# Kernel optimization log

Hardware: AMD Instinct MI355X
Metric: run time of the kernel (lower is better)

## Reference

```python
import jax, jax.numpy as jnp
import numpy as np

FP8_MAX = 448.0  # finfo(float8_e4m3fn).max
G = 128          # quantization block size


def _fp8_roundtrip(x):
    # emulate storage/rounding in float8_e4m3fn
    return x.astype(jnp.float8_e4m3fn).astype(jnp.float32)


def _quant_dequant_act(x, g=G):
    """Dynamic per-token, per-128-column-group fp8 quantization, then dequant.
    Matches fp8_act_quant: scale = amax(group)/FP8_MAX, q = clip(x/scale)."""
    lead, K = x.shape[:-1], x.shape[-1]
    xg = x.reshape(*lead, K // g, g)
    amax = jnp.max(jnp.abs(xg), axis=-1, keepdims=True)
    scale = jnp.maximum(amax, 1e-10) / FP8_MAX
    q = _fp8_roundtrip(jnp.clip(xg / scale, -FP8_MAX, FP8_MAX))
    return (q * scale).reshape(*lead, K)


def _dequant_weight(w, s, g=G):
    """Block-wise dequant: w [E,O,K] fp8 codes (stored as f32), s [E,O/g,K/g] scales."""
    E, O, K = w.shape
    wb = w.reshape(E, O // g, g, K // g, g)
    return (wb * s[:, :, None, :, None]).reshape(E, O, K)


def setup_inputs() -> dict:
    key = jax.random.key(0)
    ks = jax.random.split(key, 7)
    T, H, I, E, TK = 2048, 1024, 512, 16, 4
    hidden_states = jax.random.normal(ks[0], (T, H), dtype=jnp.float32)
    top_k_index = jax.random.randint(ks[1], (T, TK), 0, E)
    top_k_weights = jax.nn.softmax(jax.random.normal(ks[2], (T, TK), dtype=jnp.float32), axis=-1)
    # fp8-representable weight codes + positive block scale grids
    gate_up_proj = _fp8_roundtrip(jax.random.normal(ks[3], (E, 2 * I, H), dtype=jnp.float32) * 8.0)
    gate_up_proj_scale_inv = jax.random.uniform(ks[4], (E, (2 * I) // G, H // G), dtype=jnp.float32,
                                                minval=0.001, maxval=0.005)
    down_proj = _fp8_roundtrip(jax.random.normal(ks[5], (E, H, I), dtype=jnp.float32) * 8.0)
    down_proj_scale_inv = jax.random.uniform(ks[6], (E, H // G, I // G), dtype=jnp.float32,
                                             minval=0.001, maxval=0.005)
    return {
        "hidden_states": hidden_states,
        "top_k_index": top_k_index,
        "top_k_weights": top_k_weights,
        "gate_up_proj": gate_up_proj,
        "gate_up_proj_scale_inv": gate_up_proj_scale_inv,
        "down_proj": down_proj,
        "down_proj_scale_inv": down_proj_scale_inv,
    }


def reference(hidden_states, top_k_index, top_k_weights,
              gate_up_proj, gate_up_proj_scale_inv,
              down_proj, down_proj_scale_inv):
    E = gate_up_proj.shape[0]
    # dynamic activation quant (identical for every expert, since tokens are just gathered rows)
    x_deq = _quant_dequant_act(hidden_states)                       # [T, H]
    w_gu = _dequant_weight(gate_up_proj, gate_up_proj_scale_inv)    # [E, 2I, H]
    w_dn = _dequant_weight(down_proj, down_proj_scale_inv)          # [E, H, I]
    # gate_up GEMM for all experts; tokens not routed to e contribute with weight 0 below
    gate_up = jnp.einsum('th,eoh->teo', x_deq, w_gu)                # [T, E, 2I]
    gate, up = jnp.split(gate_up, 2, axis=-1)
    h = jax.nn.silu(gate) * up                                      # [T, E, I]
    h_deq = _quant_dequant_act(h)                                   # re-quantize intermediate
    expert_out = jnp.einsum('tei,ehi->teh', h_deq, w_dn)            # [T, E, H]
    # routing weight per (token, expert): sum of top_k weights whose index == e
    rw = jnp.einsum('tk,tke->te', top_k_weights,
                    jax.nn.one_hot(top_k_index, E, dtype=hidden_states.dtype))
    return jnp.einsum('teh,te->th', expert_out, rw)                 # [T, H] float32 accumulation
```

## Files before the change

kernel.cpp:

```cpp
#include <hip/hip_runtime.h>
#include <math.h>

#define T_TOK 2048
#define H_DIM 1024
#define I_DIM 512
#define N_EXP 16
#define TOPK  4
#define NPAIR (T_TOK*TOPK)

typedef unsigned short u16;
typedef __attribute__((ext_vector_type(8))) short s8v;
typedef __attribute__((ext_vector_type(4))) float f4v;

#define GLDS(g, l) __builtin_amdgcn_global_load_lds( \
    (const __attribute__((address_space(1))) void*)(g), \
    (__attribute__((address_space(3))) void*)(l), 16, 0, 0)

__device__ __forceinline__ float fp8_rt(float v) {
    float av = fabsf(v);
    if (av < 0.015625f) {
        return rintf(v * 512.0f) * 0.001953125f;
    }
    unsigned u = __float_as_uint(v);
    unsigned lsb = (u >> 20) & 1u;
    u = (u + 0x7FFFFu + lsb) & 0xFFF00000u;
    return __uint_as_float(u);
}

__device__ __forceinline__ u16 f2bf(float v) {
    return (u16)(__float_as_uint(v) >> 16);
}

__global__ void k_cvt(const float* __restrict__ in, u16* __restrict__ out, int n8) {
    int i = blockIdx.x * 256 + threadIdx.x;
    if (i >= n8) return;
    const float4* p = (const float4*)in + (size_t)i * 2;
    float4 a = p[0], b = p[1];
    int4 st;
    st.x = (int)((unsigned)f2bf(a.x) | ((unsigned)f2bf(a.y) << 16));
    st.y = (int)((unsigned)f2bf(a.z) | ((unsigned)f2bf(a.w) << 16));
    st.z = (int)((unsigned)f2bf(b.x) | ((unsigned)f2bf(b.y) << 16));
    st.w = (int)((unsigned)f2bf(b.z) | ((unsigned)f2bf(b.w) << 16));
    ((int4*)out)[i] = st;
}

__global__ void k_quant_x(const float* __restrict__ x, u16* __restrict__ xq,
                          float* __restrict__ xs) {
    int t = blockIdx.x, tid = threadIdx.x;
    float4 v = ((const float4*)(x + (size_t)t * H_DIM))[tid];
    float a = fmaxf(fmaxf(fabsf(v.x), fabsf(v.y)), fmaxf(fabsf(v.z), fabsf(v.w)));
    #pragma unroll
    for (int m = 16; m >= 1; m >>= 1) a = fmaxf(a, __shfl_xor(a, m));
    float s = fmaxf(a, 1e-10f) / 448.0f;
    ushort4 r;
    r.x = f2bf(fp8_rt(fminf(fmaxf(v.x / s, -448.f), 448.f)));
    r.y = f2bf(fp8_rt(fminf(fmaxf(v.y / s, -448.f), 448.f)));
    r.z = f2bf(fp8_rt(fminf(fmaxf(v.z / s, -448.f), 448.f)));
    r.w = f2bf(fp8_rt(fminf(fmaxf(v.w / s, -448.f), 448.f)));
    ((ushort4*)(xq + (size_t)t * H_DIM))[tid] = r;
    if ((tid & 31) == 0) xs[t * 8 + (tid >> 5)] = s;
}

__global__ void k_route(const int* __restrict__ idx, int* __restrict__ counts,
                        int* __restrict__ lists) {
    int p = blockIdx.x * 256 + threadIdx.x;
    if (p < NPAIR) {
        int e = idx[p];
        int pos = atomicAdd(&counts[e], 1);
        lists[e * NPAIR + pos] = p;
    }
}

__global__ __launch_bounds__(256, 3)
void k_gateup(const u16* __restrict__ xq, const float* __restrict__ xs,
              const int* __restrict__ counts, const int* __restrict__ lists,
              const u16* __restrict__ wgu, const float* __restrict__ sgu,
              const u16* __restrict__ zbuf, float* __restrict__ hbuf) {
    int bid = blockIdx.x;
    int e = bid & 15, tile = bid >> 4;
    int tt = tile >> 3, it = tile & 7;
    int n = counts[e];
    if (tt * 64 >= n) return;

    __shared__ __align__(16) u16 sm[2][12288];
    __shared__ float xs_l[64][8];
    __shared__ int ptok[64];

    int tid = threadIdx.x;
    int w = tid >> 6, lane = tid & 63;
    int m = w & 1, q = w >> 1;
    int l15 = lane & 15, l4 = lane >> 4;

    if (tid < 64) {
        int slot = tt * 64 + tid;
        ptok[tid] = (slot < n) ? lists[e * NPAIR + slot] : -1;
    }
    __syncthreads();
    {
        int r = tid >> 2, kb4 = (tid & 3) * 2;
        int p = ptok[r];
        xs_l[r][kb4]     = (p >= 0) ? xs[(p >> 2) * 8 + kb4]     : 0.f;
        xs_l[r][kb4 + 1] = (p >= 0) ? xs[(p >> 2) * 8 + kb4 + 1] : 0.f;
    }

    const u16* wbase = wgu + (size_t)e * 1024 * 1024;
    const u16* srcB[4];
    #pragma unroll
    for (int j = 0; j < 4; ++j) {
        int s = j * 256 + tid;
        int row = s >> 3, c = s & 7, cg = c ^ (row & 7);
        int nrow = (row < 64) ? it * 64 + row : 448 + it * 64 + row;
        srcB[j] = wbase + (size_t)nrow * H_DIM + cg * 8;
    }
    const u16* srcA[2];
    #pragma unroll
    for (int j = 0; j < 2; ++j) {
        int s = j * 256 + tid;
        int row = s >> 3, c = s & 7, cg = c ^ (row & 7);
        int p = ptok[row];
        srcA[j] = (p >= 0) ? xq + (size_t)(p >> 2) * H_DIM + cg * 8 : zbuf;
    }

    int idxA[2][2], idxB[4][2];
    #pragma unroll
    for (int fm = 0; fm < 2; ++fm) {
        int ar = m * 32 + fm * 16 + l15;
        #pragma unroll
        for (int kg = 0; kg < 2; ++kg)
            idxA[fm][kg] = 8192 + ar * 64 + (((kg * 4 + l4) ^ (ar & 7)) * 8);
    }
    #pragma unroll
    for (int nf = 0; nf < 4; ++nf) {
        int br = q * 64 + nf * 16 + l15;
        #pragma unroll
        for (int kg = 0; kg < 2; ++kg)
            idxB[nf][kg] = br * 64 + (((kg * 4 + l4) ^ (br & 7)) * 8);
    }

    auto stage = [&](int buf) {
        #pragma unroll
        for (int j = 0; j < 4; ++j) { GLDS(srcB[j], &sm[buf][j * 2048 + tid * 8]); srcB[j] += 64; }
        #pragma unroll
        for (int j = 0; j < 2; ++j) { GLDS(srcA[j], &sm[buf][8192 + j * 2048 + tid * 8]); srcA[j] += 64; }
    };

    f4v master[2][4], part[2][4];
    #pragma unroll
    for (int a = 0; a < 2; ++a)
        #pragma unroll
        for (int b = 0; b < 4; ++b) { master[a][b] = (f4v){0,0,0,0}; part[a][b] = (f4v){0,0,0,0}; }

    const float* swp = sgu + e * 64 + (q ? 4 + (it >> 1) : (it >> 1)) * 8;

    stage(0);
    __syncthreads();

    for (int t = 0; t < 16; ++t) {
        if (t < 15) stage((t + 1) & 1);
        const u16* buf = &sm[t & 1][0];
        #pragma unroll
        for (int kg = 0; kg < 2; ++kg) {
            s8v a0 = *(const s8v*)&buf[idxA[0][kg]];
            s8v a1 = *(const s8v*)&buf[idxA[1][kg]];
            #pragma unroll
            for (int nf = 0; nf < 4; ++nf) {
                s8v b = *(const s8v*)&buf[idxB[nf][kg]];
                part[0][nf] = __builtin_amdgcn_mfma_f32_16x16x32_bf16(a0, b, part[0][nf], 0, 0, 0);
                part[1][nf] = __builtin_amdgcn_mfma_f32_16x16x32_bf16(a1, b, part[1][nf], 0, 0, 0);
            }
        }
        if (t & 1) {
            int kb = t >> 1;
            float sw = swp[kb];
            #pragma unroll
            for (int fm = 0; fm < 2; ++fm) {
                float c0 = xs_l[m * 32 + fm * 16 + l4 * 4 + 0][kb] * sw;
                float c1 = xs_l[m * 32 + fm * 16 + l4 * 4 + 1][kb] * sw;
                float c2 = xs_l[m * 32 + fm * 16 + l4 * 4 + 2][kb] * sw;
                float c3 = xs_l[m * 32 + fm * 16 + l4 * 4 + 3][kb] * sw;
                #pragma unroll
                for (int nf = 0; nf < 4; ++nf) {
                    master[fm][nf][0] += c0 * part[fm][nf][0];
                    master[fm][nf][1] += c1 * part[fm][nf][1];
                    master[fm][nf][2] += c2 * part[fm][nf][2];
                    master[fm][nf][3] += c3 * part[fm][nf][3];
                    part[fm][nf] = (f4v){0,0,0,0};
                }
            }
        }
        __syncthreads();
    }

    float* Ul = (float*)sm;
    if (q == 1) {
        #pragma unroll
        for (int fm = 0; fm < 2; ++fm)
            #pragma unroll
            for (int nf = 0; nf < 4; ++nf)
                #pragma unroll
                for (int r = 0; r < 4; ++r)
                    Ul[(m * 32 + fm * 16 + l4 * 4 + r) * 65 + nf * 16 + l15] = master[fm][nf][r];
    }
    __syncthreads();
    if (q == 0) {
        #pragma unroll
        for (int fm = 0; fm < 2; ++fm)
            #pragma unroll
            for (int r = 0; r < 4; ++r) {
                int row = m * 32 + fm * 16 + l4 * 4 + r;
                int p = ptok[row];
                if (p < 0) continue;
                float* drow = hbuf + (size_t)p * I_DIM + it * 64;
                #pragma unroll
                for (int nf = 0; nf < 4; ++nf) {
                    float g = master[fm][nf][r];
                    float u = Ul[row * 65 + nf * 16 + l15];
                    drow[nf * 16 + l15] = (g / (1.0f + expf(-g))) * u;
                }
            }
    }
}

__global__ void k_quant_h(const float* __restrict__ h, u16* __restrict__ hq,
                          float* __restrict__ hs) {
    int p = blockIdx.x, tid = threadIdx.x;
    float4 v = ((const float4*)(h + (size_t)p * I_DIM))[tid];
    float a = fmaxf(fmaxf(fabsf(v.x), fabsf(v.y)), fmaxf(fabsf(v.z), fabsf(v.w)));
    #pragma unroll
    for (int m = 16; m >= 1; m >>= 1) a = fmaxf(a, __shfl_xor(a, m));
    float s = fmaxf(a, 1e-10f) / 448.0f;
    ushort4 r;
    r.x = f2bf(fp8_rt(fminf(fmaxf(v.x / s, -448.f), 448.f)));
    r.y = f2bf(fp8_rt(fminf(fmaxf(v.y / s, -448.f), 448.f)));
    r.z = f2bf(fp8_rt(fminf(fmaxf(v.z / s, -448.f), 448.f)));
    r.w = f2bf(fp8_rt(fminf(fmaxf(v.w / s, -448.f), 448.f)));
    ((ushort4*)(hq + (size_t)p * I_DIM))[tid] = r;
    if ((tid & 31) == 0) hs[p * 4 + (tid >> 5)] = s;
}

__global__ __launch_bounds__(256, 3)
void k_down(const u16* __restrict__ hq, const float* __restrict__ hs,
            const int* __restrict__ counts, const int* __restrict__ lists,
            const u16* __restrict__ wdn, const float* __restrict__ sdn,
            const float* __restrict__ tkw, const u16* __restrict__ zbuf,
            float* __restrict__ dout) {
    int bid = blockIdx.x;
    int e = bid & 15, tile = bid >> 4;
    int tt = tile >> 3, nt = tile & 7;
    int n = counts[e];
    if (tt * 64 >= n) return;

    __shared__ __align__(16) u16 sm[2][12288];
    __shared__ float hs_l[64][4];
    __shared__ float rw_l[64];
    __shared__ int ptok[64];

    int tid = threadIdx.x;
    int w = tid >> 6, lane = tid & 63;
    int m = w & 1, q = w >> 1;
    int l15 = lane & 15, l4 = lane >> 4;

    if (tid < 64) {
        int slot = tt * 64 + tid;
        ptok[tid] = (slot < n) ? lists[e * NPAIR + slot] : -1;
    }
    __syncthreads();
    {
        int r = tid >> 2, kb = tid & 3;
        int p = ptok[r];
        hs_l[r][kb] = (p >= 0) ? hs[p * 4 + kb] : 0.f;
        if (tid < 64) rw_l[tid] = (ptok[tid] >= 0) ? tkw[ptok[tid]] : 0.f;
    }

    const u16* wbase = wdn + (size_t)e * H_DIM * I_DIM;
    const u16* srcB[4];
    #pragma unroll
    for (int j = 0; j < 4; ++j) {
        int s = j * 256 + tid;
        int row = s >> 3, c = s & 7, cg = c ^ (row & 7);
        srcB[j] = wbase + (size_t)(nt * 128 + row) * I_DIM + cg * 8;
    }
    const u16* srcA[2];
    #pragma unroll
    for (int j = 0; j < 2; ++j) {
        int s = j * 256 + tid;
        int row = s >> 3, c = s & 7, cg = c ^ (row & 7);
        int p = ptok[row];
        srcA[j] = (p >= 0) ? hq + (size_t)p * I_DIM + cg * 8 : zbuf;
    }

    int idxA[2][2], idxB[4][2];
    #pragma unroll
    for (int fm = 0; fm < 2; ++fm) {
        int ar = m * 32 + fm * 16 + l15;
        #pragma unroll
        for (int kg = 0; kg < 2; ++kg)
            idxA[fm][kg] = 8192 + ar * 64 + (((kg * 4 + l4) ^ (ar & 7)) * 8);
    }
    #pragma unroll
    for (int nf = 0; nf < 4; ++nf) {
        int br = q * 64 + nf * 16 + l15;
        #pragma unroll
        for (int kg = 0; kg < 2; ++kg)
            idxB[nf][kg] = br * 64 + (((kg * 4 + l4) ^ (br & 7)) * 8);
    }

    auto stage = [&](int buf) {
        #pragma unroll
        for (int j = 0; j < 4; ++j) { GLDS(srcB[j], &sm[buf][j * 2048 + tid * 8]); srcB[j] += 64; }
        #pragma unroll
        for (int j = 0; j < 2; ++j) { GLDS(srcA[j], &sm[buf][8192 + j * 2048 + tid * 8]); srcA[j] += 64; }
    };

    f4v master[2][4], part[2][4];
    #pragma unroll
    for (int a = 0; a < 2; ++a)
        #pragma unroll
        for (int b = 0; b < 4; ++b) { master[a][b] = (f4v){0,0,0,0}; part[a][b] = (f4v){0,0,0,0}; }

    const float* swp = sdn + (e * 8 + nt) * 4;

    stage(0);
    __syncthreads();

    for (int t = 0; t < 8; ++t) {
        if (t < 7) stage((t + 1) & 1);
        const u16* buf = &sm[t & 1][0];
        #pragma unroll
        for (int kg = 0; kg < 2; ++kg) {
            s8v a0 = *(const s8v*)&buf[idxA[0][kg]];
            s8v a1 = *(const s8v*)&buf[idxA[1][kg]];
            #pragma unroll
            for (int nf = 0; nf < 4; ++nf) {
                s8v b = *(const s8v*)&buf[idxB[nf][kg]];
                part[0][nf] = __builtin_amdgcn_mfma_f32_16x16x32_bf16(a0, b, part[0][nf], 0, 0, 0);
                part[1][nf] = __builtin_amdgcn_mfma_f32_16x16x32_bf16(a1, b, part[1][nf], 0, 0, 0);
            }
        }
        if (t & 1) {
            int kb = t >> 1;
            float sw = swp[kb];
            #pragma unroll
            for (int fm = 0; fm < 2; ++fm) {
                float c0 = hs_l[m * 32 + fm * 16 + l4 * 4 + 0][kb] * sw;
                float c1 = hs_l[m * 32 + fm * 16 + l4 * 4 + 1][kb] * sw;
                float c2 = hs_l[m * 32 + fm * 16 + l4 * 4 + 2][kb] * sw;
                float c3 = hs_l[m * 32 + fm * 16 + l4 * 4 + 3][kb] * sw;
                #pragma unroll
                for (int nf = 0; nf < 4; ++nf) {
                    master[fm][nf][0] += c0 * part[fm][nf][0];
                    master[fm][nf][1] += c1 * part[fm][nf][1];
                    master[fm][nf][2] += c2 * part[fm][nf][2];
                    master[fm][nf][3] += c3 * part[fm][nf][3];
                    part[fm][nf] = (f4v){0,0,0,0};
                }
            }
        }
        __syncthreads();
    }

    #pragma unroll
    for (int fm = 0; fm < 2; ++fm)
        #pragma unroll
        for (int r = 0; r < 4; ++r) {
            int row = m * 32 + fm * 16 + l4 * 4 + r;
            int p = ptok[row];
            if (p < 0) continue;
            float rw = rw_l[row];
            float* drow = dout + (size_t)p * H_DIM + nt * 128 + q * 64;
            #pragma unroll
            for (int nf = 0; nf < 4; ++nf)
                drow[nf * 16 + l15] = rw * master[fm][nf][r];
        }
}

__global__ void k_reduce(const float* __restrict__ dout, float* __restrict__ out) {
    int i = blockIdx.x * 256 + threadIdx.x;
    int t = i >> 8, h4 = i & 255;
    const float4* d = (const float4*)dout;
    float4 a = d[(size_t)(t * 4 + 0) * 256 + h4];
    float4 b = d[(size_t)(t * 4 + 1) * 256 + h4];
    float4 c = d[(size_t)(t * 4 + 2) * 256 + h4];
    float4 e = d[(size_t)(t * 4 + 3) * 256 + h4];
    float4 r;
    r.x = a.x + b.x + c.x + e.x;
    r.y = a.y + b.y + c.y + e.y;
    r.z = a.z + b.z + c.z + e.z;
    r.w = a.w + b.w + c.w + e.w;
    ((float4*)out)[i] = r;
}

extern "C" void kernel_launch(void* const* d_in, const int* in_sizes, int n_in,
                              void* d_out, int out_size, void* d_ws, size_t ws_size,
                              hipStream_t stream) {
    const float* hs_in = (const float*)d_in[0];
    const int*   tki = (const int*)d_in[1];
    const float* tkw = (const float*)d_in[2];
    const float* wgu = (const float*)d_in[3];
    const float* sgu = (const float*)d_in[4];
    const float* wdn = (const float*)d_in[5];
    const float* sdn = (const float*)d_in[6];
    float* out = (float*)d_out;

    char* ws = (char*)d_ws;
    const size_t MB = 1024 * 1024;
    u16*   wgu_bf = (u16*)(ws);
    float* dout   = (float*)(ws);
    u16*   wdn_bf = (u16*)(ws + 32 * MB);
    u16*   xq     = (u16*)(ws + 48 * MB);
    float* xs     = (float*)(ws + 52 * MB);
    float* hbuf   = (float*)(ws + 53 * MB);
    u16*   hq     = (u16*)(ws + 69 * MB);
    float* hs     = (float*)(ws + 77 * MB);
    int*   counts = (int*)(ws + 78 * MB);
    u16*   zbuf   = (u16*)(ws + 78 * MB + 4096);
    int*   lists  = (int*)(ws + 78 * MB + 65536);

    hipMemsetAsync(counts, 0, 256, stream);
    hipMemsetAsync(zbuf, 0, 4096, stream);

    k_cvt<<<8192, 256, 0, stream>>>(wgu, wgu_bf, N_EXP * 2 * I_DIM * H_DIM / 8);
    k_cvt<<<4096, 256, 0, stream>>>(wdn, wdn_bf, N_EXP * H_DIM * I_DIM / 8);
    k_quant_x<<<T_TOK, 256, 0, stream>>>(hs_in, xq, xs);
    k_route<<<NPAIR / 256, 256, 0, stream>>>(tki, counts, lists);
    k_gateup<<<2048, 256, 0, stream>>>(xq, xs, counts, lists, wgu_bf, sgu, zbuf, hbuf);
    k_quant_h<<<NPAIR, 128, 0, stream>>>(hbuf, hq, hs);
    k_down<<<2048, 256, 0, stream>>>(hq, hs, counts, lists, wdn_bf, sdn, tkw, zbuf, dout);
    k_reduce<<<T_TOK * H_DIM / 1024, 256, 0, stream>>>(dout, out);
}
```

Baseline: 255.4 us.

## Fuse fp32-to-bf16 weight conversion into GEMM staging, drop convert kernels

Removes the standalone weight conversion kernels and instead loads fp32 weights into registers in the gate-up and down GEMMs, converting to bf16 and writing swizzled into LDS after the compute of each step. Activation tiles still use direct global-to-LDS loads. MFMA sections get raised wave priority. This avoids a full extra pass writing and re-reading converted weights, at the cost of doubling weight bytes per tile load and more registers, and redundant conversion across token tiles.

```diff
diff --git a/kernel.cpp b/kernel.cpp
--- a/kernel.cpp
+++ b/kernel.cpp
@@ -27,21 +27,8 @@
     return __uint_as_float(u);
 }
 
-__device__ __forceinline__ u16 f2bf(float v) {
-    return (u16)(__float_as_uint(v) >> 16);
-}
-
-__global__ void k_cvt(const float* __restrict__ in, u16* __restrict__ out, int n8) {
-    int i = blockIdx.x * 256 + threadIdx.x;
-    if (i >= n8) return;
-    const float4* p = (const float4*)in + (size_t)i * 2;
-    float4 a = p[0], b = p[1];
-    int4 st;
-    st.x = (int)((unsigned)f2bf(a.x) | ((unsigned)f2bf(a.y) << 16));
-    st.y = (int)((unsigned)f2bf(a.z) | ((unsigned)f2bf(a.w) << 16));
-    st.z = (int)((unsigned)f2bf(b.x) | ((unsigned)f2bf(b.y) << 16));
-    st.w = (int)((unsigned)f2bf(b.z) | ((unsigned)f2bf(b.w) << 16));
-    ((int4*)out)[i] = st;
+__device__ __forceinline__ unsigned f2bf(float v) {
+    return __float_as_uint(v) >> 16;
 }
 
 __global__ void k_quant_x(const float* __restrict__ x, u16* __restrict__ xq,
@@ -53,10 +40,10 @@
     for (int m = 16; m >= 1; m >>= 1) a = fmaxf(a, __shfl_xor(a, m));
     float s = fmaxf(a, 1e-10f) / 448.0f;
     ushort4 r;
-    r.x = f2bf(fp8_rt(fminf(fmaxf(v.x / s, -448.f), 448.f)));
-    r.y = f2bf(fp8_rt(fminf(fmaxf(v.y / s, -448.f), 448.f)));
-    r.z = f2bf(fp8_rt(fminf(fmaxf(v.z / s, -448.f), 448.f)));
-    r.w = f2bf(fp8_rt(fminf(fmaxf(v.w / s, -448.f), 448.f)));
+    r.x = (u16)f2bf(fp8_rt(fminf(fmaxf(v.x / s, -448.f), 448.f)));
+    r.y = (u16)f2bf(fp8_rt(fminf(fmaxf(v.y / s, -448.f), 448.f)));
+    r.z = (u16)f2bf(fp8_rt(fminf(fmaxf(v.z / s, -448.f), 448.f)));
+    r.w = (u16)f2bf(fp8_rt(fminf(fmaxf(v.w / s, -448.f), 448.f)));
     ((ushort4*)(xq + (size_t)t * H_DIM))[tid] = r;
     if ((tid & 31) == 0) xs[t * 8 + (tid >> 5)] = s;
 }
@@ -74,7 +61,7 @@
 __global__ __launch_bounds__(256, 3)
 void k_gateup(const u16* __restrict__ xq, const float* __restrict__ xs,
               const int* __restrict__ counts, const int* __restrict__ lists,
-              const u16* __restrict__ wgu, const float* __restrict__ sgu,
+              const float* __restrict__ wgu, const float* __restrict__ sgu,
               const u16* __restrict__ zbuf, float* __restrict__ hbuf) {
     int bid = blockIdx.x;
     int e = bid & 15, tile = bid >> 4;
@@ -103,14 +90,14 @@
         xs_l[r][kb4 + 1] = (p >= 0) ? xs[(p >> 2) * 8 + kb4 + 1] : 0.f;
     }
 
-    const u16* wbase = wgu + (size_t)e * 1024 * 1024;
-    const u16* srcB[4];
+    const float* wf = wgu + (size_t)e * (2 * I_DIM) * H_DIM;
+    int srow = tid >> 3, sc = tid & 7;
+    int nrowj[4]; int dstB[4];
     #pragma unroll
     for (int j = 0; j < 4; ++j) {
-        int s = j * 256 + tid;
-        int row = s >> 3, c = s & 7, cg = c ^ (row & 7);
-        int nrow = (row < 64) ? it * 64 + row : 448 + it * 64 + row;
-        srcB[j] = wbase + (size_t)nrow * H_DIM + cg * 8;
+        int row = j * 32 + srow;
+        nrowj[j] = (row < 64) ? it * 64 + row : 448 + it * 64 + row;
+        dstB[j] = row * 64 + (sc ^ (srow & 7)) * 8;
     }
     const u16* srcA[2];
     #pragma unroll
@@ -137,11 +124,28 @@
             idxB[nf][kg] = br * 64 + (((kg * 4 + l4) ^ (br & 7)) * 8);
     }
 
-    auto stage = [&](int buf) {
-        #pragma unroll
-        for (int j = 0; j < 4; ++j) { GLDS(srcB[j], &sm[buf][j * 2048 + tid * 8]); srcB[j] += 64; }
-        #pragma unroll
-        for (int j = 0; j < 2; ++j) { GLDS(srcA[j], &sm[buf][8192 + j * 2048 + tid * 8]); srcA[j] += 64; }
+    float4 brg[8];
+    auto loadB = [&](int ck) {
+        #pragma unroll
+        for (int j = 0; j < 4; ++j) {
+            const float4* p = (const float4*)(wf + (size_t)nrowj[j] * H_DIM + ck * 64 + sc * 8);
+            brg[2 * j] = p[0]; brg[2 * j + 1] = p[1];
+        }
+    };
+    auto writeB = [&](int buf) {
+        #pragma unroll
+        for (int j = 0; j < 4; ++j) {
+            int4 st;
+            st.x = (int)(f2bf(brg[2*j].x)   | (f2bf(brg[2*j].y)   << 16));
+            st.y = (int)(f2bf(brg[2*j].z)   | (f2bf(brg[2*j].w)   << 16));
+            st.z = (int)(f2bf(brg[2*j+1].x) | (f2bf(brg[2*j+1].y) << 16));
+            st.w = (int)(f2bf(brg[2*j+1].z) | (f2bf(brg[2*j+1].w) << 16));
+            *(int4*)&sm[buf][dstB[j]] = st;
+        }
+    };
+    auto stageA = [&](int buf, int ck) {
+        #pragma unroll
+        for (int j = 0; j < 2; ++j) GLDS(srcA[j] + ck * 64, &sm[buf][8192 + j * 2048 + tid * 8]);
     };
 
     f4v master[2][4], part[2][4];
@@ -152,12 +156,13 @@
 
     const float* swp = sgu + e * 64 + (q ? 4 + (it >> 1) : (it >> 1)) * 8;
 
-    stage(0);
+    loadB(0); stageA(0, 0); writeB(0);
     __syncthreads();
 
     for (int t = 0; t < 16; ++t) {
-        if (t < 15) stage((t + 1) & 1);
+        if (t < 15) { loadB(t + 1); stageA((t + 1) & 1, t + 1); }
         const u16* buf = &sm[t & 1][0];
+        __builtin_amdgcn_s_setprio(1);
         #pragma unroll
         for (int kg = 0; kg < 2; ++kg) {
             s8v a0 = *(const s8v*)&buf[idxA[0][kg]];
@@ -169,6 +174,7 @@
                 part[1][nf] = __builtin_amdgcn_mfma_f32_16x16x32_bf16(a1, b, part[1][nf], 0, 0, 0);
             }
         }
+        __builtin_amdgcn_s_setprio(0);
         if (t & 1) {
             int kb = t >> 1;
             float sw = swp[kb];
@@ -188,6 +194,7 @@
                 }
             }
         }
+        if (t < 15) writeB((t + 1) & 1);
         __syncthreads();
     }
 
@@ -230,10 +237,10 @@
     for (int m = 16; m >= 1; m >>= 1) a = fmaxf(a, __shfl_xor(a, m));
     float s = fmaxf(a, 1e-10f) / 448.0f;
     ushort4 r;
-    r.x = f2bf(fp8_rt(fminf(fmaxf(v.x / s, -448.f), 448.f)));
-    r.y = f2bf(fp8_rt(fminf(fmaxf(v.y / s, -448.f), 448.f)));
-    r.z = f2bf(fp8_rt(fminf(fmaxf(v.z / s, -448.f), 448.f)));
-    r.w = f2bf(fp8_rt(fminf(fmaxf(v.w / s, -448.f), 448.f)));
+    r.x = (u16)f2bf(fp8_rt(fminf(fmaxf(v.x / s, -448.f), 448.f)));
+    r.y = (u16)f2bf(fp8_rt(fminf(fmaxf(v.y / s, -448.f), 448.f)));
+    r.z = (u16)f2bf(fp8_rt(fminf(fmaxf(v.z / s, -448.f), 448.f)));
+    r.w = (u16)f2bf(fp8_rt(fminf(fmaxf(v.w / s, -448.f), 448.f)));
     ((ushort4*)(hq + (size_t)p * I_DIM))[tid] = r;
     if ((tid & 31) == 0) hs[p * 4 + (tid >> 5)] = s;
 }
@@ -241,7 +248,7 @@
 __global__ __launch_bounds__(256, 3)
 void k_down(const u16* __restrict__ hq, const float* __restrict__ hs,
             const int* __restrict__ counts, const int* __restrict__ lists,
-            const u16* __restrict__ wdn, const float* __restrict__ sdn,
+            const float* __restrict__ wdn, const float* __restrict__ sdn,
             const float* __restrict__ tkw, const u16* __restrict__ zbuf,
             float* __restrict__ dout) {
     int bid = blockIdx.x;
@@ -272,13 +279,14 @@
         if (tid < 64) rw_l[tid] = (ptok[tid] >= 0) ? tkw[ptok[tid]] : 0.f;
     }
 
-    const u16* wbase = wdn + (size_t)e * H_DIM * I_DIM;
-    const u16* srcB[4];
+    const float* wf = wdn + (size_t)e * H_DIM * I_DIM;
+    int srow = tid >> 3, sc = tid & 7;
+    int nrowj[4]; int dstB[4];
     #pragma unroll
     for (int j = 0; j < 4; ++j) {
-        int s = j * 256 + tid;
-        int row = s >> 3, c = s & 7, cg = c ^ (row & 7);
-        srcB[j] = wbase + (size_t)(nt * 128 + row) * I_DIM + cg * 8;
+        int row = j * 32 + srow;
+        nrowj[j] = nt * 128 + row;
+        dstB[j] = row * 64 + (sc ^ (srow & 7)) * 8;
     }
     const u16* srcA[2];
     #pragma unroll
@@ -305,11 +313,28 @@
             idxB[nf][kg] = br * 64 + (((kg * 4 + l4) ^ (br & 7)) * 8);
     }
 
-    auto stage = [&](int buf) {
-        #pragma unroll
-        for (int j = 0; j < 4; ++j) { GLDS(srcB[j], &sm[buf][j * 2048 + tid * 8]); srcB[j] += 64; }
-        #pragma unroll
-        for (int j = 0; j < 2; ++j) { GLDS(srcA[j], &sm[buf][8192 + j * 2048 + tid * 8]); srcA[j] += 64; }
+    float4 brg[8];
+    auto loadB = [&](int ck) {
+        #pragma unroll
+        for (int j = 0; j < 4; ++j) {
+            const float4* p = (const float4*)(wf + (size_t)nrowj[j] * I_DIM + ck * 64 + sc * 8);
+            brg[2 * j] = p[0]; brg[2 * j + 1] = p[1];
+        }
+    };
+    auto writeB = [&](int buf) {
+        #pragma unroll
+        for (int j = 0; j < 4; ++j) {
+            int4 st;
+            st.x = (int)(f2bf(brg[2*j].x)   | (f2bf(brg[2*j].y)   << 16));
+            st.y = (int)(f2bf(brg[2*j].z)   | (f2bf(brg[2*j].w)   << 16));
+            st.z = (int)(f2bf(brg[2*j+1].x) | (f2bf(brg[2*j+1].y) << 16));
+            st.w = (int)(f2bf(brg[2*j+1].z) | (f2bf(brg[2*j+1].w) << 16));
+            *(int4*)&sm[buf][dstB[j]] = st;
+        }
+    };
+    auto stageA = [&](int buf, int ck) {
+        #pragma unroll
+        for (int j = 0; j < 2; ++j) GLDS(srcA[j] + ck * 64, &sm[buf][8192 + j * 2048 + tid * 8]);
     };
 
     f4v master[2][4], part[2][4];
@@ -320,12 +345,13 @@
 
     const float* swp = sdn + (e * 8 + nt) * 4;
 
-    stage(0);
+    loadB(0); stageA(0, 0); writeB(0);
     __syncthreads();
 
     for (int t = 0; t < 8; ++t) {
-        if (t < 7) stage((t + 1) & 1);
+        if (t < 7) { loadB(t + 1); stageA((t + 1) & 1, t + 1); }
         const u16* buf = &sm[t & 1][0];
+        __builtin_amdgcn_s_setprio(1);
         #pragma unroll
         for (int kg = 0; kg < 2; ++kg) {
             s8v a0 = *(const s8v*)&buf[idxA[0][kg]];
@@ -337,6 +363,7 @@
                 part[1][nf] = __builtin_amdgcn_mfma_f32_16x16x32_bf16(a1, b, part[1][nf], 0, 0, 0);
             }
         }
+        __builtin_amdgcn_s_setprio(0);
         if (t & 1) {
             int kb = t >> 1;
             float sw = swp[kb];
@@ -356,6 +383,7 @@
                 }
             }
         }
+        if (t < 7) writeB((t + 1) & 1);
         __syncthreads();
     }
 
@@ -404,9 +432,7 @@
 
     char* ws = (char*)d_ws;
     const size_t MB = 1024 * 1024;
-    u16*   wgu_bf = (u16*)(ws);
     float* dout   = (float*)(ws);
-    u16*   wdn_bf = (u16*)(ws + 32 * MB);
     u16*   xq     = (u16*)(ws + 48 * MB);
     float* xs     = (float*)(ws + 52 * MB);
     float* hbuf   = (float*)(ws + 53 * MB);
@@ -419,12 +445,10 @@
     hipMemsetAsync(counts, 0, 256, stream);
     hipMemsetAsync(zbuf, 0, 4096, stream);
 
-    k_cvt<<<8192, 256, 0, stream>>>(wgu, wgu_bf, N_EXP * 2 * I_DIM * H_DIM / 8);
-    k_cvt<<<4096, 256, 0, stream>>>(wdn, wdn_bf, N_EXP * H_DIM * I_DIM / 8);
     k_quant_x<<<T_TOK, 256, 0, stream>>>(hs_in, xq, xs);
     k_route<<<NPAIR / 256, 256, 0, stream>>>(tki, counts, lists);
-    k_gateup<<<2048, 256, 0, stream>>>(xq, xs, counts, lists, wgu_bf, sgu, zbuf, hbuf);
+    k_gateup<<<2048, 256, 0, stream>>>(xq, xs, counts, lists, wgu, sgu, zbuf, hbuf);
     k_quant_h<<<NPAIR, 128, 0, stream>>>(hbuf, hq, hs);
-    k_down<<<2048, 256, 0, stream>>>(hq, hs, counts, lists, wdn_bf, sdn, tkw, zbuf, dout);
+    k_down<<<2048, 256, 0, stream>>>(hq, hs, counts, lists, wdn, sdn, tkw, zbuf, dout);
     k_reduce<<<T_TOK * H_DIM / 1024, 256, 0, stream>>>(dout, out);
 }
```

After: 279.0 us. 9.2% more time.

## Enlarge MoE GEMM token tile to 128 rows and merge weight conversion kernels

Applied to the files above, without the earlier changes.

The gate-up and down expert GEMM kernels now process 128 routed tokens per block instead of 64. Each wave computes a 64x64 output tile with 4x4 MFMA fragments, so weight tiles staged in LDS are reused across twice as many tokens. This halves the grid and lowers occupancy bounds to 2 blocks per CU because of higher register and LDS use. Separately, the two fp32-to-bf16 weight conversion launches are merged into one kernel that picks its source by index, saving a launch.

```diff
diff --git a/kernel.cpp b/kernel.cpp
--- a/kernel.cpp
+++ b/kernel.cpp
@@ -27,20 +27,23 @@
     return __uint_as_float(u);
 }
 
-__device__ __forceinline__ u16 f2bf(float v) {
-    return (u16)(__float_as_uint(v) >> 16);
-}
-
-__global__ void k_cvt(const float* __restrict__ in, u16* __restrict__ out, int n8) {
+__device__ __forceinline__ unsigned f2bf(float v) {
+    return __float_as_uint(v) >> 16;
+}
+
+#define N8_GU (N_EXP * 2 * I_DIM * H_DIM / 8)
+__global__ void k_cvt(const float* __restrict__ a, u16* __restrict__ oa,
+                      const float* __restrict__ b, u16* __restrict__ ob) {
     int i = blockIdx.x * 256 + threadIdx.x;
-    if (i >= n8) return;
+    const float* in = a; u16* out = oa;
+    if (i >= N8_GU) { in = b; out = ob; i -= N8_GU; }
     const float4* p = (const float4*)in + (size_t)i * 2;
-    float4 a = p[0], b = p[1];
+    float4 x = p[0], y = p[1];
     int4 st;
-    st.x = (int)((unsigned)f2bf(a.x) | ((unsigned)f2bf(a.y) << 16));
-    st.y = (int)((unsigned)f2bf(a.z) | ((unsigned)f2bf(a.w) << 16));
-    st.z = (int)((unsigned)f2bf(b.x) | ((unsigned)f2bf(b.y) << 16));
-    st.w = (int)((unsigned)f2bf(b.z) | ((unsigned)f2bf(b.w) << 16));
+    st.x = (int)(f2bf(x.x) | (f2bf(x.y) << 16));
+    st.y = (int)(f2bf(x.z) | (f2bf(x.w) << 16));
+    st.z = (int)(f2bf(y.x) | (f2bf(y.y) << 16));
+    st.w = (int)(f2bf(y.z) | (f2bf(y.w) << 16));
     ((int4*)out)[i] = st;
 }
 
@@ -53,10 +56,10 @@
     for (int m = 16; m >= 1; m >>= 1) a = fmaxf(a, __shfl_xor(a, m));
     float s = fmaxf(a, 1e-10f) / 448.0f;
     ushort4 r;
-    r.x = f2bf(fp8_rt(fminf(fmaxf(v.x / s, -448.f), 448.f)));
-    r.y = f2bf(fp8_rt(fminf(fmaxf(v.y / s, -448.f), 448.f)));
-    r.z = f2bf(fp8_rt(fminf(fmaxf(v.z / s, -448.f), 448.f)));
-    r.w = f2bf(fp8_rt(fminf(fmaxf(v.w / s, -448.f), 448.f)));
+    r.x = (u16)f2bf(fp8_rt(fminf(fmaxf(v.x / s, -448.f), 448.f)));
+    r.y = (u16)f2bf(fp8_rt(fminf(fmaxf(v.y / s, -448.f), 448.f)));
+    r.z = (u16)f2bf(fp8_rt(fminf(fmaxf(v.z / s, -448.f), 448.f)));
+    r.w = (u16)f2bf(fp8_rt(fminf(fmaxf(v.w / s, -448.f), 448.f)));
     ((ushort4*)(xq + (size_t)t * H_DIM))[tid] = r;
     if ((tid & 31) == 0) xs[t * 8 + (tid >> 5)] = s;
 }
@@ -71,7 +74,7 @@
     }
 }
 
-__global__ __launch_bounds__(256, 3)
+__global__ __launch_bounds__(256, 2)
 void k_gateup(const u16* __restrict__ xq, const float* __restrict__ xs,
               const int* __restrict__ counts, const int* __restrict__ lists,
               const u16* __restrict__ wgu, const float* __restrict__ sgu,
@@ -80,27 +83,28 @@
     int e = bid & 15, tile = bid >> 4;
     int tt = tile >> 3, it = tile & 7;
     int n = counts[e];
-    if (tt * 64 >= n) return;
-
-    __shared__ __align__(16) u16 sm[2][12288];
-    __shared__ float xs_l[64][8];
-    __shared__ int ptok[64];
+    if (tt * 128 >= n) return;
+
+    __shared__ __align__(16) u16 sm[2][16384];
+    __shared__ float xs_l[128][8];
+    __shared__ int ptok[128];
 
     int tid = threadIdx.x;
     int w = tid >> 6, lane = tid & 63;
-    int m = w & 1, q = w >> 1;
+    int wr = w & 1, wc = w >> 1;
     int l15 = lane & 15, l4 = lane >> 4;
 
-    if (tid < 64) {
-        int slot = tt * 64 + tid;
+    if (tid < 128) {
+        int slot = tt * 128 + tid;
         ptok[tid] = (slot < n) ? lists[e * NPAIR + slot] : -1;
     }
     __syncthreads();
     {
-        int r = tid >> 2, kb4 = (tid & 3) * 2;
+        int base = tid * 4, r = base >> 3, kb = base & 7;
         int p = ptok[r];
-        xs_l[r][kb4]     = (p >= 0) ? xs[(p >> 2) * 8 + kb4]     : 0.f;
-        xs_l[r][kb4 + 1] = (p >= 0) ? xs[(p >> 2) * 8 + kb4 + 1] : 0.f;
+        #pragma unroll
+        for (int i = 0; i < 4; ++i)
+            xs_l[r][kb + i] = (p >= 0) ? xs[(p >> 2) * 8 + kb + i] : 0.f;
     }
 
     const u16* wbase = wgu + (size_t)e * 1024 * 1024;
@@ -112,79 +116,78 @@
         int nrow = (row < 64) ? it * 64 + row : 448 + it * 64 + row;
         srcB[j] = wbase + (size_t)nrow * H_DIM + cg * 8;
     }
-    const u16* srcA[2];
-    #pragma unroll
-    for (int j = 0; j < 2; ++j) {
+    const u16* srcA[4];
+    #pragma unroll
+    for (int j = 0; j < 4; ++j) {
         int s = j * 256 + tid;
         int row = s >> 3, c = s & 7, cg = c ^ (row & 7);
         int p = ptok[row];
         srcA[j] = (p >= 0) ? xq + (size_t)(p >> 2) * H_DIM + cg * 8 : zbuf;
     }
 
-    int idxA[2][2], idxB[4][2];
-    #pragma unroll
-    for (int fm = 0; fm < 2; ++fm) {
-        int ar = m * 32 + fm * 16 + l15;
+    int idxA[4][2], idxB[4][2];
+    #pragma unroll
+    for (int fr = 0; fr < 4; ++fr) {
+        int ar = wr * 64 + fr * 16 + l15;
         #pragma unroll
         for (int kg = 0; kg < 2; ++kg)
-            idxA[fm][kg] = 8192 + ar * 64 + (((kg * 4 + l4) ^ (ar & 7)) * 8);
-    }
-    #pragma unroll
-    for (int nf = 0; nf < 4; ++nf) {
-        int br = q * 64 + nf * 16 + l15;
+            idxA[fr][kg] = 8192 + ar * 64 + (((kg * 4 + l4) ^ (ar & 7)) * 8);
+    }
+    #pragma unroll
+    for (int nc = 0; nc < 4; ++nc) {
+        int br = wc * 64 + nc * 16 + l15;
         #pragma unroll
         for (int kg = 0; kg < 2; ++kg)
-            idxB[nf][kg] = br * 64 + (((kg * 4 + l4) ^ (br & 7)) * 8);
-    }
-
-    auto stage = [&](int buf) {
-        #pragma unroll
-        for (int j = 0; j < 4; ++j) { GLDS(srcB[j], &sm[buf][j * 2048 + tid * 8]); srcB[j] += 64; }
-        #pragma unroll
-        for (int j = 0; j < 2; ++j) { GLDS(srcA[j], &sm[buf][8192 + j * 2048 + tid * 8]); srcA[j] += 64; }
+            idxB[nc][kg] = br * 64 + (((kg * 4 + l4) ^ (br & 7)) * 8);
+    }
+
+    auto stage = [&](int buf, int ck) {
+        #pragma unroll
+        for (int j = 0; j < 4; ++j) GLDS(srcB[j] + ck * 64, &sm[buf][(j * 256 + tid) * 8]);
+        #pragma unroll
+        for (int j = 0; j < 4; ++j) GLDS(srcA[j] + ck * 64, &sm[buf][8192 + (j * 256 + tid) * 8]);
     };
 
-    f4v master[2][4], part[2][4];
-    #pragma unroll
-    for (int a = 0; a < 2; ++a)
+    f4v master[4][4], part[4][4];
+    #pragma unroll
+    for (int a = 0; a < 4; ++a)
         #pragma unroll
         for (int b = 0; b < 4; ++b) { master[a][b] = (f4v){0,0,0,0}; part[a][b] = (f4v){0,0,0,0}; }
 
-    const float* swp = sgu + e * 64 + (q ? 4 + (it >> 1) : (it >> 1)) * 8;
-
-    stage(0);
+    const float* swp = sgu + e * 64 + (wc ? 4 + (it >> 1) : (it >> 1)) * 8;
+
+    stage(0, 0);
     __syncthreads();
 
     for (int t = 0; t < 16; ++t) {
-        if (t < 15) stage((t + 1) & 1);
+        if (t < 15) stage((t + 1) & 1, t + 1);
         const u16* buf = &sm[t & 1][0];
         #pragma unroll
         for (int kg = 0; kg < 2; ++kg) {
-            s8v a0 = *(const s8v*)&buf[idxA[0][kg]];
-            s8v a1 = *(const s8v*)&buf[idxA[1][kg]];
-            #pragma unroll
-            for (int nf = 0; nf < 4; ++nf) {
-                s8v b = *(const s8v*)&buf[idxB[nf][kg]];
-                part[0][nf] = __builtin_amdgcn_mfma_f32_16x16x32_bf16(a0, b, part[0][nf], 0, 0, 0);
-                part[1][nf] = __builtin_amdgcn_mfma_f32_16x16x32_bf16(a1, b, part[1][nf], 0, 0, 0);
+            s8v a[4];
+            #pragma unroll
+            for (int fr = 0; fr < 4; ++fr) a[fr] = *(const s8v*)&buf[idxA[fr][kg]];
+            #pragma unroll
+            for (int nc = 0; nc < 4; ++nc) {
+                s8v b = *(const s8v*)&buf[idxB[nc][kg]];
+                #pragma unroll
+                for (int fr = 0; fr < 4; ++fr)
+                    part[fr][nc] = __builtin_amdgcn_mfma_f32_16x16x32_bf16(a[fr], b, part[fr][nc], 0, 0, 0);
             }
         }
         if (t & 1) {
             int kb = t >> 1;
             float sw = swp[kb];
             #pragma unroll
-            for (int fm = 0; fm < 2; ++fm) {
-                float c0 = xs_l[m * 32 + fm * 16 + l4 * 4 + 0][kb] * sw;
-                float c1 = xs_l[m * 32 + fm * 16 + l4 * 4 + 1][kb] * sw;
-                float c2 = xs_l[m * 32 + fm * 16 + l4 * 4 + 2][kb] * sw;
-                float c3 = xs_l[m * 32 + fm * 16 + l4 * 4 + 3][kb] * sw;
-                #pragma unroll
-                for (int nf = 0; nf < 4; ++nf) {
-                    master[fm][nf][0] += c0 * part[fm][nf][0];
-                    master[fm][nf][1] += c1 * part[fm][nf][1];
-                    master[fm][nf][2] += c2 * part[fm][nf][2];
-                    master[fm][nf][3] += c3 * part[fm][nf][3];
-                    part[fm][nf] = (f4v){0,0,0,0};
+            for (int fr = 0; fr < 4; ++fr) {
+                #pragma unroll
+                for (int r = 0; r < 4; ++r) {
+                    float c = xs_l[wr * 64 + fr * 16 + l4 * 4 + r][kb] * sw;
+                    #pragma unroll
+                    for (int nc = 0; nc < 4; ++nc) {
+                        master[fr][nc][r] += c * part[fr][nc][r];
+                        part[fr][nc][r] = 0.f;
+                    }
                 }
             }
         }
@@ -192,30 +195,30 @@
     }
 
     float* Ul = (float*)sm;
-    if (q == 1) {
-        #pragma unroll
-        for (int fm = 0; fm < 2; ++fm)
-            #pragma unroll
-            for (int nf = 0; nf < 4; ++nf)
+    if (wc == 1) {
+        #pragma unroll
+        for (int fr = 0; fr < 4; ++fr)
+            #pragma unroll
+            for (int nc = 0; nc < 4; ++nc)
                 #pragma unroll
                 for (int r = 0; r < 4; ++r)
-                    Ul[(m * 32 + fm * 16 + l4 * 4 + r) * 65 + nf * 16 + l15] = master[fm][nf][r];
+                    Ul[(wr * 64 + fr * 16 + l4 * 4 + r) * 66 + nc * 16 + l15] = master[fr][nc][r];
     }
     __syncthreads();
-    if (q == 0) {
-        #pragma unroll
-        for (int fm = 0; fm < 2; ++fm)
+    if (wc == 0) {
+        #pragma unroll
+        for (int fr = 0; fr < 4; ++fr)
             #pragma unroll
             for (int r = 0; r < 4; ++r) {
-                int row = m * 32 + fm * 16 + l4 * 4 + r;
+                int row = wr * 64 + fr * 16 + l4 * 4 + r;
                 int p = ptok[row];
                 if (p < 0) continue;
                 float* drow = hbuf + (size_t)p * I_DIM + it * 64;
                 #pragma unroll
-                for (int nf = 0; nf < 4; ++nf) {
-                    float g = master[fm][nf][r];
-                    float u = Ul[row * 65 + nf * 16 + l15];
-                    drow[nf * 16 + l15] = (g / (1.0f + expf(-g))) * u;
+                for (int nc = 0; nc < 4; ++nc) {
+                    float g = master[fr][nc][r];
+                    float u = Ul[row * 66 + nc * 16 + l15];
+                    drow[nc * 16 + l15] = (g / (1.0f + expf(-g))) * u;
                 }
             }
     }
@@ -230,15 +233,15 @@
     for (int m = 16; m >= 1; m >>= 1) a = fmaxf(a, __shfl_xor(a, m));
     float s = fmaxf(a, 1e-10f) / 448.0f;
     ushort4 r;
-    r.x = f2bf(fp8_rt(fminf(fmaxf(v.x / s, -448.f), 448.f)));
-    r.y = f2bf(fp8_rt(fminf(fmaxf(v.y / s, -448.f), 448.f)));
-    r.z = f2bf(fp8_rt(fminf(fmaxf(v.z / s, -448.f), 448.f)));
-    r.w = f2bf(fp8_rt(fminf(fmaxf(v.w / s, -448.f), 448.f)));
+    r.x = (u16)f2bf(fp8_rt(fminf(fmaxf(v.x / s, -448.f), 448.f)));
+    r.y = (u16)f2bf(fp8_rt(fminf(fmaxf(v.y / s, -448.f), 448.f)));
+    r.z = (u16)f2bf(fp8_rt(fminf(fmaxf(v.z / s, -448.f), 448.f)));
+    r.w = (u16)f2bf(fp8_rt(fminf(fmaxf(v.w / s, -448.f), 448.f)));
     ((ushort4*)(hq + (size_t)p * I_DIM))[tid] = r;
     if ((tid & 31) == 0) hs[p * 4 + (tid >> 5)] = s;
 }
 
-__global__ __launch_bounds__(256, 3)
+__global__ __launch_bounds__(256, 2)
 void k_down(const u16* __restrict__ hq, const float* __restrict__ hs,
             const int* __restrict__ counts, const int* __restrict__ lists,
             const u16* __restrict__ wdn, const float* __restrict__ sdn,
@@ -248,28 +251,29 @@
     int e = bid & 15, tile = bid >> 4;
     int tt = tile >> 3, nt = tile & 7;
     int n = counts[e];
-    if (tt * 64 >= n) return;
-
-    __shared__ __align__(16) u16 sm[2][12288];
-    __shared__ float hs_l[64][4];
-    __shared__ float rw_l[64];
-    __shared__ int ptok[64];
+    if (tt * 128 >= n) return;
+
+    __shared__ __align__(16) u16 sm[2][16384];
+    __shared__ float hs_l[128][4];
+    __shared__ float rw_l[128];
+    __shared__ int ptok[128];
 
     int tid = threadIdx.x;
     int w = tid >> 6, lane = tid & 63;
-    int m = w & 1, q = w >> 1;
+    int wr = w & 1, wc = w >> 1;
     int l15 = lane & 15, l4 = lane >> 4;
 
-    if (tid < 64) {
-        int slot = tt * 64 + tid;
+    if (tid < 128) {
+        int slot = tt * 128 + tid;
         ptok[tid] = (slot < n) ? lists[e * NPAIR + slot] : -1;
     }
     __syncthreads();
     {
-        int r = tid >> 2, kb = tid & 3;
+        int base = tid * 2, r = base >> 2, kb = base & 3;
         int p = ptok[r];
-        hs_l[r][kb] = (p >= 0) ? hs[p * 4 + kb] : 0.f;
-        if (tid < 64) rw_l[tid] = (ptok[tid] >= 0) ? tkw[ptok[tid]] : 0.f;
+        hs_l[r][kb]     = (p >= 0) ? hs[p * 4 + kb]     : 0.f;
+        hs_l[r][kb + 1] = (p >= 0) ? hs[p * 4 + kb + 1] : 0.f;
+        if (tid < 128) rw_l[tid] = (ptok[tid] >= 0) ? tkw[ptok[tid]] : 0.f;
     }
 
     const u16* wbase = wdn + (size_t)e * H_DIM * I_DIM;
@@ -280,79 +284,78 @@
         int row = s >> 3, c = s & 7, cg = c ^ (row & 7);
         srcB[j] = wbase + (size_t)(nt * 128 + row) * I_DIM + cg * 8;
     }
-    const u16* srcA[2];
-    #pragma unroll
-    for (int j = 0; j < 2; ++j) {
+    const u16* srcA[4];
+    #pragma unroll
+    for (int j = 0; j < 4; ++j) {
         int s = j * 256 + tid;
         int row = s >> 3, c = s & 7, cg = c ^ (row & 7);
         int p = ptok[row];
         srcA[j] = (p >= 0) ? hq + (size_t)p * I_DIM + cg * 8 : zbuf;
     }
 
-    int idxA[2][2], idxB[4][2];
-    #pragma unroll
-    for (int fm = 0; fm < 2; ++fm) {
-        int ar = m * 32 + fm * 16 + l15;
+    int idxA[4][2], idxB[4][2];
+    #pragma unroll
+    for (int fr = 0; fr < 4; ++fr) {
+        int ar = wr * 64 + fr * 16 + l15;
         #pragma unroll
         for (int kg = 0; kg < 2; ++kg)
-            idxA[fm][kg] = 8192 + ar * 64 + (((kg * 4 + l4) ^ (ar & 7)) * 8);
-    }
-    #pragma unroll
-    for (int nf = 0; nf < 4; ++nf) {
-        int br = q * 64 + nf * 16 + l15;
+            idxA[fr][kg] = 8192 + ar * 64 + (((kg * 4 + l4) ^ (ar & 7)) * 8);
+    }
+    #pragma unroll
+    for (int nc = 0; nc < 4; ++nc) {
+        int br = wc * 64 + nc * 16 + l15;
         #pragma unroll
         for (int kg = 0; kg < 2; ++kg)
-            idxB[nf][kg] = br * 64 + (((kg * 4 + l4) ^ (br & 7)) * 8);
-    }
-
-    auto stage = [&](int buf) {
-        #pragma unroll
-        for (int j = 0; j < 4; ++j) { GLDS(srcB[j], &sm[buf][j * 2048 + tid * 8]); srcB[j] += 64; }
-        #pragma unroll
-        for (int j = 0; j < 2; ++j) { GLDS(srcA[j], &sm[buf][8192 + j * 2048 + tid * 8]); srcA[j] += 64; }
+            idxB[nc][kg] = br * 64 + (((kg * 4 + l4) ^ (br & 7)) * 8);
+    }
+
+    auto stage = [&](int buf, int ck) {
+        #pragma unroll
+        for (int j = 0; j < 4; ++j) GLDS(srcB[j] + ck * 64, &sm[buf][(j * 256 + tid) * 8]);
+        #pragma unroll
+        for (int j = 0; j < 4; ++j) GLDS(srcA[j] + ck * 64, &sm[buf][8192 + (j * 256 + tid) * 8]);
     };
 
-    f4v master[2][4], part[2][4];
-    #pragma unroll
-    for (int a = 0; a < 2; ++a)
+    f4v master[4][4], part[4][4];
+    #pragma unroll
+    for (int a = 0; a < 4; ++a)
         #pragma unroll
         for (int b = 0; b < 4; ++b) { master[a][b] = (f4v){0,0,0,0}; part[a][b] = (f4v){0,0,0,0}; }
 
     const float* swp = sdn + (e * 8 + nt) * 4;
 
-    stage(0);
+    stage(0, 0);
     __syncthreads();
 
     for (int t = 0; t < 8; ++t) {
-        if (t < 7) stage((t + 1) & 1);
+        if (t < 7) stage((t + 1) & 1, t + 1);
         const u16* buf = &sm[t & 1][0];
         #pragma unroll
         for (int kg = 0; kg < 2; ++kg) {
-            s8v a0 = *(const s8v*)&buf[idxA[0][kg]];
-            s8v a1 = *(const s8v*)&buf[idxA[1][kg]];
-            #pragma unroll
-            for (int nf = 0; nf < 4; ++nf) {
-                s8v b = *(const s8v*)&buf[idxB[nf][kg]];
-                part[0][nf] = __builtin_amdgcn_mfma_f32_16x16x32_bf16(a0, b, part[0][nf], 0, 0, 0);
-                part[1][nf] = __builtin_amdgcn_mfma_f32_16x16x32_bf16(a1, b, part[1][nf], 0, 0, 0);
+            s8v a[4];
+            #pragma unroll
+            for (int fr = 0; fr < 4; ++fr) a[fr] = *(const s8v*)&buf[idxA[fr][kg]];
+            #pragma unroll
+            for (int nc = 0; nc < 4; ++nc) {
+                s8v b = *(const s8v*)&buf[idxB[nc][kg]];
+                #pragma unroll
+                for (int fr = 0; fr < 4; ++fr)
+                    part[fr][nc] = __builtin_amdgcn_mfma_f32_16x16x32_bf16(a[fr], b, part[fr][nc], 0, 0, 0);
             }
         }
         if (t & 1) {
             int kb = t >> 1;
             float sw = swp[kb];
             #pragma unroll
-            for (int fm = 0; fm < 2; ++fm) {
-                float c0 = hs_l[m * 32 + fm * 16 + l4 * 4 + 0][kb] * sw;
-                float c1 = hs_l[m * 32 + fm * 16 + l4 * 4 + 1][kb] * sw;
-                float c2 = hs_l[m * 32 + fm * 16 + l4 * 4 + 2][kb] * sw;
-                float c3 = hs_l[m * 32 + fm * 16 + l4 * 4 + 3][kb] * sw;
-                #pragma unroll
-                for (int nf = 0; nf < 4; ++nf) {
-                    master[fm][nf][0] += c0 * part[fm][nf][0];
-                    master[fm][nf][1] += c1 * part[fm][nf][1];
-                    master[fm][nf][2] += c2 * part[fm][nf][2];
-                    master[fm][nf][3] += c3 * part[fm][nf][3];
-                    part[fm][nf] = (f4v){0,0,0,0};
+            for (int fr = 0; fr < 4; ++fr) {
+                #pragma unroll
+                for (int r = 0; r < 4; ++r) {
+                    float c = hs_l[wr * 64 + fr * 16 + l4 * 4 + r][kb] * sw;
+                    #pragma unroll
+                    for (int nc = 0; nc < 4; ++nc) {
+                        master[fr][nc][r] += c * part[fr][nc][r];
+                        part[fr][nc][r] = 0.f;
+                    }
                 }
             }
         }
@@ -360,17 +363,17 @@
     }
 
     #pragma unroll
-    for (int fm = 0; fm < 2; ++fm)
+    for (int fr = 0; fr < 4; ++fr)
         #pragma unroll
         for (int r = 0; r < 4; ++r) {
-            int row = m * 32 + fm * 16 + l4 * 4 + r;
+            int row = wr * 64 + fr * 16 + l4 * 4 + r;
             int p = ptok[row];
             if (p < 0) continue;
             float rw = rw_l[row];
-            float* drow = dout + (size_t)p * H_DIM + nt * 128 + q * 64;
-            #pragma unroll
-            for (int nf = 0; nf < 4; ++nf)
-                drow[nf * 16 + l15] = rw * master[fm][nf][r];
+            float* drow = dout + (size_t)p * H_DIM + nt * 128 + wc * 64;
+            #pragma unroll
+            for (int nc = 0; nc < 4; ++nc)
+                drow[nc * 16 + l15] = rw * master[fr][nc][r];
         }
 }
 
@@ -419,12 +422,11 @@
     hipMemsetAsync(counts, 0, 256, stream);
     hipMemsetAsync(zbuf, 0, 4096, stream);
 
-    k_cvt<<<8192, 256, 0, stream>>>(wgu, wgu_bf, N_EXP * 2 * I_DIM * H_DIM / 8);
-    k_cvt<<<4096, 256, 0, stream>>>(wdn, wdn_bf, N_EXP * H_DIM * I_DIM / 8);
+    k_cvt<<<12288, 256, 0, stream>>>(wgu, wgu_bf, wdn, wdn_bf);
     k_quant_x<<<T_TOK, 256, 0, stream>>>(hs_in, xq, xs);
     k_route<<<NPAIR / 256, 256, 0, stream>>>(tki, counts, lists);
-    k_gateup<<<2048, 256, 0, stream>>>(xq, xs, counts, lists, wgu_bf, sgu, zbuf, hbuf);
+    k_gateup<<<1024, 256, 0, stream>>>(xq, xs, counts, lists, wgu_bf, sgu, zbuf, hbuf);
     k_quant_h<<<NPAIR, 128, 0, stream>>>(hbuf, hq, hs);
-    k_down<<<2048, 256, 0, stream>>>(hq, hs, counts, lists, wdn_bf, sdn, tkw, zbuf, dout);
+    k_down<<<1024, 256, 0, stream>>>(hq, hs, counts, lists, wdn_bf, sdn, tkw, zbuf, dout);
     k_reduce<<<T_TOK * H_DIM / 1024, 256, 0, stream>>>(dout, out);
 }
```

New measurement: 273.4 us. +7.0%, slower.
